# Kernel optimization log

Hardware: AMD Instinct MI355X
Metric: run time of the kernel (lower is better)

The kernel has to match this reference:

```python
import jax, jax.numpy as jnp
import numpy as np

B, T, D_IN = 32, 512, 1024
D_HID = 512
D_CODE = 1024
K = 256  # codebook size
COMMIT = 0.25
LAMBDA_MMD = 0.5
LN_EPS = 1e-5


def setup_inputs() -> dict:
    key = jax.random.key(0)
    ks = jax.random.split(key, 20)
    def w(k, shape, scale=0.02):
        return jax.random.normal(k, shape, dtype=jnp.float32) * scale
    inp = {
        "x": jax.random.normal(ks[0], (B, T, D_IN), dtype=jnp.float32),
        "prior": jax.random.normal(ks[1], (B, D_CODE), dtype=jnp.float32),
        # encoder: Linear(1024,512) -> LN(512) -> ReLU -> Linear(512,1024)
        "enc_W1": w(ks[2], (D_IN, D_HID)), "enc_b1": jnp.zeros((D_HID,), jnp.float32),
        "ln_g": jnp.ones((D_HID,), jnp.float32), "ln_b": jnp.zeros((D_HID,), jnp.float32),
        "enc_W2": w(ks[3], (D_HID, D_CODE)), "enc_b2": jnp.zeros((D_CODE,), jnp.float32),
        # codebook, init uniform(-1/K, 1/K) like the torch module
        "codebook": jax.random.uniform(ks[4], (K, D_CODE), jnp.float32, -1.0 / K, 1.0 / K),
        # projector: Linear(1024,512) -> ReLU -> Linear(512,1024)
        "proj_W1": w(ks[5], (D_CODE, D_HID)), "proj_b1": jnp.zeros((D_HID,), jnp.float32),
        "proj_W2": w(ks[6], (D_HID, D_CODE)), "proj_b2": jnp.zeros((D_CODE,), jnp.float32),
        # GRU(1024 -> 1024), torch gate order (r, z, n)
        "gru_Wih": w(ks[7], (D_CODE, 3 * D_CODE)), "gru_Whh": w(ks[8], (D_CODE, 3 * D_CODE)),
        "gru_bih": jnp.zeros((3 * D_CODE,), jnp.float32), "gru_bhh": jnp.zeros((3 * D_CODE,), jnp.float32),
        # head: Linear(1024, 1024)
        "head_W": w(ks[9], (D_CODE, D_IN)), "head_b": jnp.zeros((D_IN,), jnp.float32),
    }
    return inp


def _gaussian_kernel(a, b):
    # exp(-cdist(a,b)^2 / dim)
    d = a.shape[1]
    sq = (jnp.sum(a * a, 1, keepdims=True) + jnp.sum(b * b, 1)[None, :]
          - 2.0 * a @ b.T)
    sq = jnp.maximum(sq, 0.0)
    return jnp.exp(-sq / d)


def _gru(quantized, Wih, Whh, bih, bhh):
    # quantized: [B, T, D]; precompute input projections, scan over time
    gx = jnp.einsum("btd,de->bte", quantized, Wih) + bih  # [B,T,3D]
    gx = jnp.swapaxes(gx, 0, 1)  # [T,B,3D]
    h0 = jnp.zeros((quantized.shape[0], Whh.shape[0]), quantized.dtype)

    def step(h, gxt):
        gh = h @ Whh + bhh
        xr, xz, xn = jnp.split(gxt, 3, axis=-1)
        hr, hz, hn = jnp.split(gh, 3, axis=-1)
        r = jax.nn.sigmoid(xr + hr)
        z = jax.nn.sigmoid(xz + hz)
        n = jnp.tanh(xn + r * hn)
        h_new = (1.0 - z) * n + z * h
        return h_new, h_new

    _, hs = jax.lax.scan(step, h0, gx)  # [T,B,D]
    return jnp.swapaxes(hs, 0, 1)  # [B,T,D]


def reference(x, prior, enc_W1, enc_b1, ln_g, ln_b, enc_W2, enc_b2, codebook,
              proj_W1, proj_b1, proj_W2, proj_b2,
              gru_Wih, gru_Whh, gru_bih, gru_bhh, head_W, head_b):
    # ---- encoder ----
    h = x @ enc_W1 + enc_b1
    mu = jnp.mean(h, -1, keepdims=True)
    var = jnp.mean((h - mu) ** 2, -1, keepdims=True)
    h = (h - mu) * jax.lax.rsqrt(var + LN_EPS) * ln_g + ln_b
    h = jax.nn.relu(h)
    features = h @ enc_W2 + enc_b2  # [B,T,D_CODE]

    # ---- vector quantizer ----
    flat = features.reshape(-1, D_CODE)  # [B*T, D]
    dist = (jnp.sum(flat * flat, 1, keepdims=True) + jnp.sum(codebook * codebook, 1)
            - 2.0 * flat @ codebook.T)  # [B*T, K]
    idx = jnp.argmin(dist, axis=1)  # [B*T]
    quantized = codebook[idx].reshape(features.shape)
    e_latent = jnp.mean((jax.lax.stop_gradient(quantized) - features) ** 2)
    q_latent = jnp.mean((quantized - jax.lax.stop_gradient(features)) ** 2)
    vq_loss = q_latent + COMMIT * e_latent
    quantized = features + jax.lax.stop_gradient(quantized - features)  # straight-through

    # ---- projector + MMD ----
    p = jax.nn.relu(quantized @ proj_W1 + proj_b1)
    aligned = p @ proj_W2 + proj_b2  # [B,T,D]
    xm = jnp.mean(aligned, axis=1)  # [B,D]
    xx = _gaussian_kernel(xm, xm).mean()
    yy = _gaussian_kernel(prior, prior).mean()
    xy = _gaussian_kernel(xm, prior).mean()
    mmd = xx + yy - 2.0 * xy

    # ---- GRU decoder + head ----
    context = _gru(quantized, gru_Wih, gru_Whh, gru_bih, gru_bhh)
    recon = context @ head_W + head_b  # [B,T,D_IN]
    recon_loss = jnp.mean((recon - x) ** 2)

    total = recon_loss + vq_loss + LAMBDA_MMD * mmd
    return jnp.stack([recon_loss, vq_loss, mmd, total])
```

## Files before the change

### kernel.cpp

```cpp
#include <hip/hip_runtime.h>


typedef __attribute__((ext_vector_type(4))) float  f32x4;
typedef __attribute__((ext_vector_type(8))) short  s16x8;
typedef __attribute__((ext_vector_type(4))) short  s16x4;
typedef __attribute__((ext_vector_type(8))) __bf16 bf16x8;
typedef unsigned long long u64;
typedef unsigned int       u32;

__device__ __forceinline__ short f2bf(float f) {
  __bf16 h = (__bf16)f;
  return __builtin_bit_cast(short, h);
}
__device__ __forceinline__ float bf2f(short s) {
  return (float)__builtin_bit_cast(__bf16, s);
}
__device__ __forceinline__ f32x4 mfma16(s16x8 a, s16x8 b, f32x4 c) {
  return __builtin_amdgcn_mfma_f32_16x16x32_bf16(
      __builtin_bit_cast(bf16x8, a), __builtin_bit_cast(bf16x8, b), c, 0, 0, 0);
}
__device__ __forceinline__ void vm_drain() {
  asm volatile("s_waitcnt vmcnt(0)" ::: "memory");
}
__device__ __forceinline__ void st_uc32(u32* p, u32 v) {
  __hip_atomic_store(p, v, __ATOMIC_RELAXED, __HIP_MEMORY_SCOPE_AGENT);
}

template<bool AF32, int EPI>
__global__ __launch_bounds__(256)
void gemm_k(const void* __restrict__ Ap, const float* __restrict__ Bp,
            const float* __restrict__ bias, void* __restrict__ Cp,
            const float* __restrict__ Xref, float* __restrict__ accum,
            int M, int N, int K)
{
  __shared__ short As[128][72];
  __shared__ short Bs[128][72];
  const int tid  = threadIdx.x;
  const long bm  = (long)blockIdx.x * 128;
  const long bn  = (long)blockIdx.y * 128;
  const int wave = tid >> 6, lane = tid & 63;
  const int wm = (wave >> 1) * 64, wn = (wave & 1) * 64;
  const int l16 = lane & 15, quad = lane >> 4;

  f32x4 acc[4][4];
#pragma unroll
  for (int i = 0; i < 4; ++i)
#pragma unroll
    for (int j = 0; j < 4; ++j) acc[i][j] = (f32x4){0.f, 0.f, 0.f, 0.f};

  const int atc = tid & 15, atr = tid >> 4;
  const int btc = tid & 31, btr = tid >> 5;

  for (int kt = 0; kt < K; kt += 64) {
#pragma unroll
    for (int p = 0; p < 8; ++p) {
      int r = p * 16 + atr;
      if (AF32) {
        const float* src = (const float*)Ap + (bm + r) * (long)K + kt + atc * 4;
        f32x4 v = *(const f32x4*)src;
        s16x4 s;
        s.x = f2bf(v.x); s.y = f2bf(v.y); s.z = f2bf(v.z); s.w = f2bf(v.w);
        *(s16x4*)&As[r][atc * 4] = s;
      } else {
        const short* src = (const short*)Ap + (bm + r) * (long)K + kt + atc * 4;
        *(s16x4*)&As[r][atc * 4] = *(const s16x4*)src;
      }
    }
#pragma unroll
    for (int p = 0; p < 8; ++p) {
      int kk = p * 8 + btr;
      const float* brow = Bp + (long)(kt + kk) * N + bn + btc;
#pragma unroll
      for (int j = 0; j < 4; ++j) Bs[btc + 32 * j][kk] = f2bf(brow[32 * j]);
    }
    __syncthreads();
#pragma unroll
    for (int kk = 0; kk < 64; kk += 32) {
      s16x8 af[4], bf[4];
#pragma unroll
      for (int i = 0; i < 4; ++i)
        af[i] = *(const s16x8*)&As[wm + i * 16 + l16][kk + quad * 8];
#pragma unroll
      for (int j = 0; j < 4; ++j)
        bf[j] = *(const s16x8*)&Bs[wn + j * 16 + l16][kk + quad * 8];
#pragma unroll
      for (int i = 0; i < 4; ++i)
#pragma unroll
        for (int j = 0; j < 4; ++j) acc[i][j] = mfma16(af[i], bf[j], acc[i][j]);
    }
    __syncthreads();
  }

  if (EPI == 3) {
    float ls = 0.f;
#pragma unroll
    for (int i = 0; i < 4; ++i)
#pragma unroll
      for (int j = 0; j < 4; ++j) {
        long col = bn + wn + j * 16 + l16;
        float bv = bias[col];
#pragma unroll
        for (int r = 0; r < 4; ++r) {
          long row = bm + wm + i * 16 + quad * 4 + r;
          float v = acc[i][j][r] + bv;
          float d = v - Xref[row * N + col];
          ls += d * d;
        }
      }
#pragma unroll
    for (int off = 32; off > 0; off >>= 1) ls += __shfl_xor(ls, off, 64);
    if (lane == 0) atomicAdd(accum, ls);
  } else {
#pragma unroll
    for (int i = 0; i < 4; ++i)
#pragma unroll
      for (int j = 0; j < 4; ++j) {
        long col = bn + wn + j * 16 + l16;
        float bv = bias[col];
#pragma unroll
        for (int r = 0; r < 4; ++r) {
          long row = bm + wm + i * 16 + quad * 4 + r;
          float v = acc[i][j][r] + bv;
          if (EPI == 2) v = fmaxf(v, 0.f);
          if (EPI == 0) ((float*)Cp)[row * N + col] = v;
          else          ((short*)Cp)[row * N + col] = f2bf(v);
        }
      }
  }
}

__global__ __launch_bounds__(256)
void ln_relu_k(const float* __restrict__ hp, const float* __restrict__ g,
               const float* __restrict__ b, short* __restrict__ out)
{
  const int wave = threadIdx.x >> 6, lane = threadIdx.x & 63;
  const long row = (long)blockIdx.x * 4 + wave;
  const float* hr = hp + row * 512;
  const int c0 = lane * 4, c1 = 256 + lane * 4;
  f32x4 v0 = *(const f32x4*)(hr + c0);
  f32x4 v1 = *(const f32x4*)(hr + c1);
  float s  = v0.x + v0.y + v0.z + v0.w + v1.x + v1.y + v1.z + v1.w;
  float ss = v0.x*v0.x + v0.y*v0.y + v0.z*v0.z + v0.w*v0.w
           + v1.x*v1.x + v1.y*v1.y + v1.z*v1.z + v1.w*v1.w;
#pragma unroll
  for (int off = 32; off > 0; off >>= 1) {
    s  += __shfl_xor(s, off, 64);
    ss += __shfl_xor(ss, off, 64);
  }
  float mu  = s * (1.f / 512.f);
  float var = ss * (1.f / 512.f) - mu * mu;
  float rs  = rsqrtf(var + 1e-5f);
  f32x4 g0 = *(const f32x4*)(g + c0), bb0 = *(const f32x4*)(b + c0);
  f32x4 g1 = *(const f32x4*)(g + c1), bb1 = *(const f32x4*)(b + c1);
  s16x4 o0, o1;
#pragma unroll
  for (int e = 0; e < 4; ++e) {
    o0[e] = f2bf(fmaxf((v0[e] - mu) * rs * g0[e] + bb0[e], 0.f));
    o1[e] = f2bf(fmaxf((v1[e] - mu) * rs * g1[e] + bb1[e], 0.f));
  }
  *(s16x4*)(out + row * 512 + c0) = o0;
  *(s16x4*)(out + row * 512 + c1) = o1;
}

__global__ __launch_bounds__(256)
void prep_cb_k(const float* __restrict__ cb, float* __restrict__ cbT,
               float* __restrict__ cbBias)
{
  __shared__ float red[256];
  const int r = blockIdx.x, tid = threadIdx.x;
  const float* row = cb + (long)r * 1024;
  float ss = 0.f;
  for (int c = tid; c < 1024; c += 256) {
    float v = row[c];
    cbT[(long)c * 256 + r] = v;
    ss += v * v;
  }
  red[tid] = ss; __syncthreads();
  for (int st = 128; st > 0; st >>= 1) {
    if (tid < st) red[tid] += red[tid + st];
    __syncthreads();
  }
  if (tid == 0) cbBias[r] = -0.5f * red[0];
}

__global__ __launch_bounds__(256)
void vq_k(const float* __restrict__ sc, const short* __restrict__ feat,
          int* __restrict__ idxp, float* __restrict__ e_acc)
{
  __shared__ float ep[4];
  const int wave = threadIdx.x >> 6, lane = threadIdx.x & 63;
  const long row = (long)blockIdx.x * 4 + wave;
  f32x4 s = *(const f32x4*)(sc + row * 256 + lane * 4);
  float best = s.x; int bi = lane * 4;
  if (s.y > best) { best = s.y; bi = lane * 4 + 1; }
  if (s.z > best) { best = s.z; bi = lane * 4 + 2; }
  if (s.w > best) { best = s.w; bi = lane * 4 + 3; }
#pragma unroll
  for (int off = 32; off > 0; off >>= 1) {
    float ov = __shfl_xor(best, off, 64);
    int   oi = __shfl_xor(bi, off, 64);
    if (ov > best || (ov == best && oi < bi)) { best = ov; bi = oi; }
  }
  const short* fr = feat + row * 1024;
  float sq = 0.f;
#pragma unroll
  for (int p = 0; p < 2; ++p) {
    s16x8 v = *(const s16x8*)(fr + p * 512 + lane * 8);
#pragma unroll
    for (int e = 0; e < 8; ++e) { float f = bf2f(v[e]); sq += f * f; }
  }
#pragma unroll
  for (int off = 32; off > 0; off >>= 1) sq += __shfl_xor(sq, off, 64);
  if (lane == 0) { idxp[row] = bi; ep[wave] = sq - 2.f * best; }
  __syncthreads();
  if (threadIdx.x == 0) atomicAdd(e_acc, ep[0] + ep[1] + ep[2] + ep[3]);
}

__global__ __launch_bounds__(256)
void hist_xm_k(const int* __restrict__ idxp, const float* __restrict__ AC,
               float* __restrict__ xm)
{
  __shared__ int   hist[256];
  __shared__ float hf[256];
  const int b = blockIdx.x, tid = threadIdx.x;
  hist[tid] = 0; __syncthreads();
  for (int t = tid; t < 512; t += 256) atomicAdd(&hist[idxp[b * 512 + t]], 1);
  __syncthreads();
  hf[tid] = (float)hist[tid] * (1.f / 512.f);
  __syncthreads();
  for (int d = tid; d < 1024; d += 256) {
    float a = 0.f;
    for (int k = 0; k < 256; ++k) a += hf[k] * AC[(long)k * 1024 + d];
    xm[(long)b * 1024 + d] = a;
  }
}

__global__ __launch_bounds__(1024)
void mmd_k(const float* __restrict__ xm, const float* __restrict__ prior,
           float* __restrict__ mmd_out)
{
  extern __shared__ float xs[];
  __shared__ float red[48];
  const int tid = threadIdx.x;
  for (int i = tid; i < 32 * 1024; i += 1024)
    xs[(i >> 10) * 1028 + (i & 1023)] = xm[i];
  __syncthreads();
  const int i = tid >> 5, j = tid & 31;
  const float* xi = xs + i * 1028;
  const float* xj = xs + j * 1028;
  const float* pi = prior + (long)i * 1024;
  const float* pj = prior + (long)j * 1024;
  float dxx = 0.f, dyy = 0.f, dxy = 0.f;
  for (int d = 0; d < 1024; d += 4) {
    f32x4 a = *(const f32x4*)(xi + d);
    f32x4 b = *(const f32x4*)(xj + d);
    f32x4 p = *(const f32x4*)(pi + d);
    f32x4 q = *(const f32x4*)(pj + d);
#pragma unroll
    for (int e = 0; e < 4; ++e) {
      float t1 = a[e] - b[e]; dxx += t1 * t1;
      float t2 = p[e] - q[e]; dyy += t2 * t2;
      float t3 = a[e] - q[e]; dxy += t3 * t3;
    }
  }
  float kxx = __expf(-dxx * (1.f / 1024.f));
  float kyy = __expf(-dyy * (1.f / 1024.f));
  float kxy = __expf(-dxy * (1.f / 1024.f));
  const int wv = tid >> 6, lane = tid & 63;
#pragma unroll
  for (int off = 32; off > 0; off >>= 1) {
    kxx += __shfl_xor(kxx, off, 64);
    kyy += __shfl_xor(kyy, off, 64);
    kxy += __shfl_xor(kxy, off, 64);
  }
  if (lane == 0) { red[wv] = kxx; red[16 + wv] = kyy; red[32 + wv] = kxy; }
  __syncthreads();
  if (tid == 0) {
    float sxx = 0.f, syy = 0.f, sxy = 0.f;
    for (int w = 0; w < 16; ++w) {
      sxx += red[w]; syy += red[16 + w]; sxy += red[32 + w];
    }
    mmd_out[0] = (sxx + syy - 2.f * sxy) * (1.f / 1024.f);
  }
}

__global__ __launch_bounds__(128, 1)
void gru_k(const float* __restrict__ Whh, const float* __restrict__ bhh,
           const float* __restrict__ cgx, const int* __restrict__ idxp,
           u32* __restrict__ ctxw, const short* __restrict__ ctxr,
           int* __restrict__ flags)
{
  extern __shared__ short Bsl[];
  const int tid = threadIdx.x, g = blockIdx.x;
  const int wave = tid >> 6, lane = tid & 63;
  const int l16 = lane & 15, quad = lane >> 4;

  for (int i = tid; i < 48 * 1024; i += 128) {
    int c = i % 48, k = i / 48;
    int gate = c >> 4, dl = c & 15;
    Bsl[c * 1034 + k] = f2bf(Whh[(long)k * 3072 + gate * 1024 + g * 16 + dl]);
  }
  const int dcol = g * 16 + l16;
  const float bhr = bhh[dcol], bhz = bhh[dcol + 1024], bhn = bhh[dcol + 2048];
  const short* b0 = &Bsl[l16 * 1034 + quad * 8];
  const short* b1 = b0 + 16 * 1034;
  const short* b2 = b0 + 32 * 1034;
  float hreg[4] = {0.f, 0.f, 0.f, 0.f};
  int brow[4];
#pragma unroll
  for (int r = 0; r < 4; ++r) brow[r] = wave * 16 + quad * 4 + r;
  const int myflag = g * 2 + wave;
  __syncthreads();

  const long arow = ((long)(wave * 16 + l16) * 512) * 1024 + quad * 8;

  float xr[4], xz[4], xn[4];
#pragma unroll
  for (int r = 0; r < 4; ++r) {
    int code = idxp[brow[r] * 512];
    const float* gp = cgx + (long)code * 3072 + dcol;
    xr[r] = gp[0]; xz[r] = gp[1024]; xn[r] = gp[2048];
  }

  for (int t = 0; t < 512; ++t) {
    f32x4 ar_ = {0.f,0.f,0.f,0.f}, az = ar_, an = ar_;
    if (t > 0) {
      int a, b;
      do {
        a = __hip_atomic_load(&flags[lane],      __ATOMIC_RELAXED,
                              __HIP_MEMORY_SCOPE_AGENT);
        b = __hip_atomic_load(&flags[64 + lane], __ATOMIC_RELAXED,
                              __HIP_MEMORY_SCOPE_AGENT);
      } while (__any(a < t || b < t));
      asm volatile("" ::: "memory");
      const short* ap = ctxr + arow + (long)(t - 1) * 1024;
      s16x8 A[32];
#pragma unroll
      for (int ks = 0; ks < 32; ++ks)
        A[ks] = __builtin_nontemporal_load((const s16x8*)(ap + ks * 32));
      asm volatile("" ::: "memory");
#pragma unroll
      for (int ks = 0; ks < 32; ++ks) {
        ar_ = mfma16(A[ks], *(const s16x8*)(b0 + ks * 32), ar_);
        az  = mfma16(A[ks], *(const s16x8*)(b1 + ks * 32), az);
        an  = mfma16(A[ks], *(const s16x8*)(b2 + ks * 32), an);
      }
    }
#pragma unroll
    for (int r = 0; r < 4; ++r) {
      float rr = 1.f / (1.f + __expf(-(xr[r] + ar_[r] + bhr)));
      float zz = 1.f / (1.f + __expf(-(xz[r] + az[r] + bhz)));
      float u  = xn[r] + rr * (an[r] + bhn);
      float e  = __expf(-2.f * u);
      float nn = (1.f - e) / (1.f + e);
      hreg[r]  = (1.f - zz) * nn + zz * hreg[r];
    }
    int tn = (t + 1 < 512) ? t + 1 : 0;
#pragma unroll
    for (int r = 0; r < 4; ++r) {
      int code = idxp[brow[r] * 512 + tn];
      const float* gp = cgx + (long)code * 3072 + dcol;
      xr[r] = gp[0]; xz[r] = gp[1024]; xn[r] = gp[2048];
    }
#pragma unroll
    for (int r = 0; r < 4; ++r) {
      unsigned short hb = (unsigned short)f2bf(hreg[r]);
      u32 other = (u32)__shfl_xor((int)hb, 1, 64) & 0xffffu;
      if ((l16 & 1) == 0) {
        u32 w = (u32)hb | (other << 16);
        st_uc32(ctxw + ((long)brow[r] * 512 + t) * 512 + (dcol >> 1), w);
      }
    }
    vm_drain();
    if (lane == 0)
      __hip_atomic_store(&flags[myflag], t + 1, __ATOMIC_RELAXED,
                         __HIP_MEMORY_SCOPE_AGENT);
  }
}

__global__ void fin_k(const float* __restrict__ scal, float* __restrict__ out)
{
  float recon = scal[3] * (1.f / 16777216.f);
  float vq    = 1.25f * scal[2] * (1.f / 16777216.f);
  float mmd   = scal[4];
  out[0] = recon;
  out[1] = vq;
  out[2] = mmd;
  out[3] = recon + vq + 0.5f * mmd;
}

extern "C" void kernel_launch(void* const* d_in, const int* in_sizes, int n_in,
                              void* d_out, int out_size, void* d_ws, size_t ws_size,
                              hipStream_t stream)
{
  const float* x     = (const float*)d_in[0];
  const float* prior = (const float*)d_in[1];
  const float* encW1 = (const float*)d_in[2];
  const float* encb1 = (const float*)d_in[3];
  const float* lng   = (const float*)d_in[4];
  const float* lnb   = (const float*)d_in[5];
  const float* encW2 = (const float*)d_in[6];
  const float* encb2 = (const float*)d_in[7];
  const float* cb    = (const float*)d_in[8];
  const float* pW1   = (const float*)d_in[9];
  const float* pb1   = (const float*)d_in[10];
  const float* pW2   = (const float*)d_in[11];
  const float* pb2   = (const float*)d_in[12];
  const float* Wih   = (const float*)d_in[13];
  const float* Whh   = (const float*)d_in[14];
  const float* bih   = (const float*)d_in[15];
  const float* bhh   = (const float*)d_in[16];
  const float* headW = (const float*)d_in[17];
  const float* headb = (const float*)d_in[18];

  char* ws = (char*)d_ws;
  if (ws_size < 89654528) return;
  float* h_pre  = (float*)(ws + 0);
  float* scores = h_pre;
  int*   flags  = (int*)(ws + 131072);
  short* h1     = (short*)(ws + 33554432);
  short* feat   = (short*)(ws + 50331648);
  u32*   ctxw   = (u32*)feat;
  short* ctxr   = feat;
  float* cgx    = (float*)(ws + 83886080);
  float* AC     = (float*)(ws + 87031808);
  float* cbT    = (float*)(ws + 88080384);
  short* ch     = (short*)(ws + 89128960);
  float* xm     = (float*)(ws + 89391104);
  int*   idxp   = (int*)  (ws + 89522176);
  float* scal   = (float*)(ws + 89653248);
  float* e_acc  = scal + 2;
  float* r_acc  = scal + 3;
  float* mmdv   = scal + 4;
  float* cbBias = (float*)(ws + 89653504);

  hipMemsetAsync(scal, 0, 256, stream);

  dim3 blk(256);
  prep_cb_k<<<256, blk, 0, stream>>>(cb, cbT, cbBias);
  gemm_k<true, 0><<<dim3(128, 4), blk, 0, stream>>>(
      x, encW1, encb1, h_pre, nullptr, nullptr, 16384, 512, 1024);
  ln_relu_k<<<4096, blk, 0, stream>>>(h_pre, lng, lnb, h1);
  gemm_k<false, 1><<<dim3(128, 8), blk, 0, stream>>>(
      h1, encW2, encb2, feat, nullptr, nullptr, 16384, 1024, 512);
  gemm_k<false, 0><<<dim3(128, 2), blk, 0, stream>>>(
      feat, cbT, cbBias, scores, nullptr, nullptr, 16384, 256, 1024);
  vq_k<<<4096, blk, 0, stream>>>(scores, feat, idxp, e_acc);
  hipMemsetAsync(flags, 0, 512, stream);
  gemm_k<true, 2><<<dim3(2, 4), blk, 0, stream>>>(
      cb, pW1, pb1, ch, nullptr, nullptr, 256, 512, 1024);
  gemm_k<false, 0><<<dim3(2, 8), blk, 0, stream>>>(
      ch, pW2, pb2, AC, nullptr, nullptr, 256, 1024, 512);
  gemm_k<true, 0><<<dim3(2, 24), blk, 0, stream>>>(
      cb, Wih, bih, cgx, nullptr, nullptr, 256, 3072, 1024);
  hist_xm_k<<<32, blk, 0, stream>>>(idxp, AC, xm);
  mmd_k<<<1, 1024, 32 * 1028 * 4, stream>>>(xm, prior, mmdv);
  gru_k<<<64, 128, 48 * 1034 * 2, stream>>>(Whh, bhh, cgx, idxp,
                                            ctxw, ctxr, flags);
  gemm_k<false, 3><<<dim3(128, 8), blk, 0, stream>>>(
      ctxr, headW, headb, nullptr, x, r_acc, 16384, 1024, 1024);
  fin_k<<<1, 1, 0, stream>>>(scal, (float*)d_out);
}
```

Baseline: 5.922 ms.

## Replace GRU flag barrier with step-tagged hidden-state words in double buffer

The persistent GRU kernel no longer waits on per-block flags after draining its stores. Each block now writes the hidden state as 64-bit words holding the bf16 pair plus the timestep tag into a two-slot buffer. Readers poll those words directly until every tag reaches the needed step, then feed the data straight to the MFMAs. This removes the vmcnt drain and the separate flag round trip on the serial critical path. The cost is doubled load traffic per step, 128 u64 registers per lane, repeated full reloads while spinning, and an LDS transpose to pack the words.

```diff
diff --git a/kernel.cpp b/kernel.cpp
--- a/kernel.cpp
+++ b/kernel.cpp
@@ -5,6 +5,7 @@
 typedef __attribute__((ext_vector_type(8))) short  s16x8;
 typedef __attribute__((ext_vector_type(4))) short  s16x4;
 typedef __attribute__((ext_vector_type(8))) __bf16 bf16x8;
+typedef __attribute__((ext_vector_type(4))) unsigned int u32x4;
 typedef unsigned long long u64;
 typedef unsigned int       u32;
 
@@ -18,12 +19,6 @@
 __device__ __forceinline__ f32x4 mfma16(s16x8 a, s16x8 b, f32x4 c) {
   return __builtin_amdgcn_mfma_f32_16x16x32_bf16(
       __builtin_bit_cast(bf16x8, a), __builtin_bit_cast(bf16x8, b), c, 0, 0, 0);
-}
-__device__ __forceinline__ void vm_drain() {
-  asm volatile("s_waitcnt vmcnt(0)" ::: "memory");
-}
-__device__ __forceinline__ void st_uc32(u32* p, u32 v) {
-  __hip_atomic_store(p, v, __ATOMIC_RELAXED, __HIP_MEMORY_SCOPE_AGENT);
 }
 
 template<bool AF32, int EPI>
@@ -287,10 +282,10 @@
 __global__ __launch_bounds__(128, 1)
 void gru_k(const float* __restrict__ Whh, const float* __restrict__ bhh,
            const float* __restrict__ cgx, const int* __restrict__ idxp,
-           u32* __restrict__ ctxw, const short* __restrict__ ctxr,
-           int* __restrict__ flags)
+           u64* __restrict__ hx, u32* __restrict__ ctxw)
 {
   extern __shared__ short Bsl[];
+  short* scr = Bsl + 48 * 1034;
   const int tid = threadIdx.x, g = blockIdx.x;
   const int wave = tid >> 6, lane = tid & 63;
   const int l16 = lane & 15, quad = lane >> 4;
@@ -305,14 +300,13 @@
   const short* b0 = &Bsl[l16 * 1034 + quad * 8];
   const short* b1 = b0 + 16 * 1034;
   const short* b2 = b0 + 32 * 1034;
+  short* sw = scr + wave * 320;
   float hreg[4] = {0.f, 0.f, 0.f, 0.f};
   int brow[4];
 #pragma unroll
   for (int r = 0; r < 4; ++r) brow[r] = wave * 16 + quad * 4 + r;
-  const int myflag = g * 2 + wave;
-  __syncthreads();
-
-  const long arow = ((long)(wave * 16 + l16) * 512) * 1024 + quad * 8;
+  const int myrow = wave * 16 + l16;
+  __syncthreads();
 
   float xr[4], xz[4], xn[4];
 #pragma unroll
@@ -325,25 +319,35 @@
   for (int t = 0; t < 512; ++t) {
     f32x4 ar_ = {0.f,0.f,0.f,0.f}, az = ar_, an = ar_;
     if (t > 0) {
-      int a, b;
+      const u64* hb = hx + ((long)(((t - 1) & 1) * 32 + myrow)) * 512 + quad * 4;
+      u64 A2[128];
+      const int tmin = t - 1;
+      int att = 0, ok;
       do {
-        a = __hip_atomic_load(&flags[lane],      __ATOMIC_RELAXED,
-                              __HIP_MEMORY_SCOPE_AGENT);
-        b = __hip_atomic_load(&flags[64 + lane], __ATOMIC_RELAXED,
-                              __HIP_MEMORY_SCOPE_AGENT);
-      } while (__any(a < t || b < t));
-      asm volatile("" ::: "memory");
-      const short* ap = ctxr + arow + (long)(t - 1) * 1024;
-      s16x8 A[32];
-#pragma unroll
-      for (int ks = 0; ks < 32; ++ks)
-        A[ks] = __builtin_nontemporal_load((const s16x8*)(ap + ks * 32));
-      asm volatile("" ::: "memory");
+        if (att++) __builtin_amdgcn_s_sleep(1);
+#pragma unroll
+        for (int ks = 0; ks < 32; ++ks)
+#pragma unroll
+          for (int i = 0; i < 4; ++i)
+            A2[ks * 4 + i] = __hip_atomic_load(hb + ks * 16 + i,
+                                 __ATOMIC_RELAXED, __HIP_MEMORY_SCOPE_AGENT);
+        int mn = 0x7fffffff;
+#pragma unroll
+        for (int u = 0; u < 128; ++u) {
+          int tg = (int)(u32)(A2[u] >> 32);
+          mn = tg < mn ? tg : mn;
+        }
+        ok = __all(mn >= tmin);
+      } while (!ok);
 #pragma unroll
       for (int ks = 0; ks < 32; ++ks) {
-        ar_ = mfma16(A[ks], *(const s16x8*)(b0 + ks * 32), ar_);
-        az  = mfma16(A[ks], *(const s16x8*)(b1 + ks * 32), az);
-        an  = mfma16(A[ks], *(const s16x8*)(b2 + ks * 32), an);
+        u32x4 aw;
+        aw.x = (u32)A2[ks * 4 + 0]; aw.y = (u32)A2[ks * 4 + 1];
+        aw.z = (u32)A2[ks * 4 + 2]; aw.w = (u32)A2[ks * 4 + 3];
+        s16x8 a8 = __builtin_bit_cast(s16x8, aw);
+        ar_ = mfma16(a8, *(const s16x8*)(b0 + ks * 32), ar_);
+        az  = mfma16(a8, *(const s16x8*)(b1 + ks * 32), az);
+        an  = mfma16(a8, *(const s16x8*)(b2 + ks * 32), an);
       }
     }
 #pragma unroll
@@ -355,6 +359,25 @@
       float nn = (1.f - e) / (1.f + e);
       hreg[r]  = (1.f - zz) * nn + zz * hreg[r];
     }
+    s16x4 hv;
+    hv.x = f2bf(hreg[0]); hv.y = f2bf(hreg[1]);
+    hv.z = f2bf(hreg[2]); hv.w = f2bf(hreg[3]);
+    *(s16x4*)(sw + l16 * 20 + quad * 4) = hv;
+    asm volatile("s_waitcnt lgkmcnt(0)" ::: "memory");
+    __builtin_amdgcn_wave_barrier();
+#pragma unroll
+    for (int s = 0; s < 2; ++s) {
+      int u = lane + 64 * s;
+      int row_loc = u & 15, cp = u >> 4;
+      u32 v0 = (unsigned short)sw[(2 * cp) * 20 + row_loc];
+      u32 v1 = (unsigned short)sw[(2 * cp + 1) * 20 + row_loc];
+      u32 dat = v0 | (v1 << 16);
+      u64 unit = (u64)dat | ((u64)(u32)t << 32);
+      int rg = wave * 16 + row_loc;
+      __hip_atomic_store(hx + ((long)((t & 1) * 32 + rg)) * 512 + g * 8 + cp,
+                         unit, __ATOMIC_RELAXED, __HIP_MEMORY_SCOPE_AGENT);
+      ctxw[((long)rg * 512 + t) * 512 + g * 8 + cp] = dat;
+    }
     int tn = (t + 1 < 512) ? t + 1 : 0;
 #pragma unroll
     for (int r = 0; r < 4; ++r) {
@@ -362,19 +385,6 @@
       const float* gp = cgx + (long)code * 3072 + dcol;
       xr[r] = gp[0]; xz[r] = gp[1024]; xn[r] = gp[2048];
     }
-#pragma unroll
-    for (int r = 0; r < 4; ++r) {
-      unsigned short hb = (unsigned short)f2bf(hreg[r]);
-      u32 other = (u32)__shfl_xor((int)hb, 1, 64) & 0xffffu;
-      if ((l16 & 1) == 0) {
-        u32 w = (u32)hb | (other << 16);
-        st_uc32(ctxw + ((long)brow[r] * 512 + t) * 512 + (dcol >> 1), w);
-      }
-    }
-    vm_drain();
-    if (lane == 0)
-      __hip_atomic_store(&flags[myflag], t + 1, __ATOMIC_RELAXED,
-                         __HIP_MEMORY_SCOPE_AGENT);
   }
 }
 
@@ -417,7 +427,7 @@
   if (ws_size < 89654528) return;
   float* h_pre  = (float*)(ws + 0);
   float* scores = h_pre;
-  int*   flags  = (int*)(ws + 131072);
+  u64*   hx     = (u64*)(ws + 0);
   short* h1     = (short*)(ws + 33554432);
   short* feat   = (short*)(ws + 50331648);
   u32*   ctxw   = (u32*)feat;
@@ -446,7 +456,7 @@
   gemm_k<false, 0><<<dim3(128, 2), blk, 0, stream>>>(
       feat, cbT, cbBias, scores, nullptr, nullptr, 16384, 256, 1024);
   vq_k<<<4096, blk, 0, stream>>>(scores, feat, idxp, e_acc);
-  hipMemsetAsync(flags, 0, 512, stream);
+  hipMemsetAsync(ws, 0xFF, 262144, stream);
   gemm_k<true, 2><<<dim3(2, 4), blk, 0, stream>>>(
       cb, pW1, pb1, ch, nullptr, nullptr, 256, 512, 1024);
   gemm_k<false, 0><<<dim3(2, 8), blk, 0, stream>>>(
@@ -455,8 +465,8 @@
       cb, Wih, bih, cgx, nullptr, nullptr, 256, 3072, 1024);
   hist_xm_k<<<32, blk, 0, stream>>>(idxp, AC, xm);
   mmd_k<<<1, 1024, 32 * 1028 * 4, stream>>>(xm, prior, mmdv);
-  gru_k<<<64, 128, 48 * 1034 * 2, stream>>>(Whh, bhh, cgx, idxp,
-                                            ctxw, ctxr, flags);
+  gru_k<<<64, 128, (48 * 1034 + 2 * 320) * 2, stream>>>(
+      Whh, bhh, cgx, idxp, hx, ctxw);
   gemm_k<false, 3><<<dim3(128, 8), blk, 0, stream>>>(
       ctxr, headW, headb, nullptr, x, r_acc, 16384, 1024, 1024);
   fin_k<<<1, 1, 0, stream>>>(scal, (float*)d_out);
```

Result: slower. 10.10 ms (+70.5%).
